# Kernel tuning notes

Hardware: AMD Instinct MI355X
Metric: run time of the kernel (lower is better)

## Reference

```python
import jax, jax.numpy as jnp
import numpy as np

K = 10          # hardcoded in module (self.K = 10)
H = 26          # neighbors per query point in this run
PAD_H = 28      # layer_ind2neighbor[layer_ind=0]
KP_EXTENT = 1.2 # linear-influence extent


def setup_inputs() -> dict:
    key = jax.random.key(0)
    ks = jax.random.split(key, 6)
    N, Ns, Cin, Cout = 65536, 65536, 64, 128
    q_pts = jax.random.normal(ks[0], (N, 3), jnp.float32)
    s_pts = jax.random.normal(ks[1], (Ns, 3), jnp.float32)
    neighb_inds = jax.random.randint(ks[2], (N, H), 0, Ns)
    x = jax.random.normal(ks[3], (Ns, Cin), jnp.float32)
    # kernel_points_generator: Linear(PAD_H*3 -> K*3)
    gen_W = jax.random.normal(ks[4], (K * 3, PAD_H * 3), jnp.float32) * (1.0 / np.sqrt(PAD_H * 3))
    gen_b = jnp.zeros((K * 3,), jnp.float32)
    # KPConv weights: [K, in, out] (kaiming_uniform in torch; scaled normal here)
    weights = jax.random.normal(ks[5], (K, Cin, Cout), jnp.float32) * (1.0 / np.sqrt(Cin))
    return {"q_pts": q_pts, "s_pts": s_pts, "x": x,
            "gen_W": gen_W, "gen_b": gen_b, "weights": weights,
            "neighb_inds": neighb_inds}


def _kpconv(q_pts, s_pts, x, gen_W, gen_b, weights, neighb_inds):
    N = q_pts.shape[0]
    # shadow support point far away (index Ns)
    s_pad = jnp.concatenate([s_pts, jnp.full((1, 3), 1e6, s_pts.dtype)], axis=0)
    neighbors = s_pad[neighb_inds] - q_pts[:, None, :]                          # [N,H,3]
    # generative kernel points: pad neighbor list with -1 up to PAD_H, run linear
    padded = jnp.concatenate(
        [neighbors, jnp.full((N, PAD_H - H, 3), -1.0, neighbors.dtype)], axis=1)
    kp = (padded.reshape(N, -1) @ gen_W.T + gen_b).reshape(N, 1, K, 3)          # [N,1,K,3]
    diff = neighbors[:, :, None, :] - kp                                        # [N,H,K,3]
    sq_d = jnp.sum(diff * diff, axis=3)                                         # [N,H,K]
    # KP_influence == 'linear'
    all_w = jnp.maximum(1.0 - jnp.sqrt(sq_d) / KP_EXTENT, 0.0)
    all_w = jnp.swapaxes(all_w, 1, 2)                                           # [N,K,H]
    # shadow feature row (zeros) at index Ns
    x_pad = jnp.concatenate([x, jnp.zeros((1, x.shape[1]), x.dtype)], axis=0)
    neighb_x = x_pad[neighb_inds]                                               # [N,H,Cin]
    weighted = jnp.einsum('nkh,nhi->nki', all_w, neighb_x)                      # [N,K,Cin]
    return jnp.einsum('nki,kio->no', weighted, weights)                         # [N,Cout]


def reference(q_pts, s_pts, x, gen_W, gen_b, weights, neighb_inds):
    return _kpconv(q_pts, s_pts, x, gen_W, gen_b, weights, neighb_inds)
```

## Files before the change

### kernel.cpp

```cpp
#include <hip/hip_runtime.h>
#include <stdint.h>

#define N_Q   65536
#define N_S   65536
#define NB_H  26
#define PAD_H 28
#define KP    10
#define CIN   64
#define COUT  128
#define MT    8
#define BM    64

typedef unsigned short u16x4  __attribute__((ext_vector_type(4)));
typedef unsigned short u16x8  __attribute__((ext_vector_type(8)));
typedef float          f32x4  __attribute__((ext_vector_type(4)));
typedef _Float16       f16x8  __attribute__((ext_vector_type(8)));
typedef _Float16       f16x2  __attribute__((ext_vector_type(2)));

#define CVT_BLOCKS 2049
#define PACK_BLOCKS 40

static __device__ __forceinline__ unsigned short f2h(float f) {
  return __builtin_bit_cast(unsigned short, (_Float16)f);
}

static __device__ __forceinline__ unsigned int pkrtz_u32(float a, float b) {
  return __builtin_bit_cast(unsigned int, __builtin_amdgcn_cvt_pkrtz(a, b));
}

static __device__ __forceinline__ float fdot2u(unsigned int a, unsigned int b, float c) {
#if __has_builtin(__builtin_amdgcn_fdot2)
  return __builtin_amdgcn_fdot2(__builtin_bit_cast(f16x2, a),
                                __builtin_bit_cast(f16x2, b), c, false);
#else
  f16x2 ha = __builtin_bit_cast(f16x2, a), hb = __builtin_bit_cast(f16x2, b);
  return c + (float)ha[0] * (float)hb[0] + (float)ha[1] * (float)hb[1];
#endif
}

__global__ void prep_kernel(const float* __restrict__ x,
                            const float* __restrict__ w,
                            unsigned short* __restrict__ xh,
                            unsigned short* __restrict__ bp) {
  if (blockIdx.x < CVT_BLOCKS) {
    long t = (long)blockIdx.x * blockDim.x + threadIdx.x;
    long off = t * 8;
    if (off >= (long)(N_S + 1) * CIN) return;
    u16x8 o;
    if (off < (long)N_S * CIN) {
      f32x4 a = *(const f32x4*)(x + off);
      f32x4 b = *(const f32x4*)(x + off + 4);
      o[0] = f2h(a[0]); o[1] = f2h(a[1]); o[2] = f2h(a[2]); o[3] = f2h(a[3]);
      o[4] = f2h(b[0]); o[5] = f2h(b[1]); o[6] = f2h(b[2]); o[7] = f2h(b[3]);
    } else {
      o = (u16x8)0;
    }
    *(u16x8*)(xh + off) = o;
  } else {
    int t = (blockIdx.x - CVT_BLOCKS) * blockDim.x + threadIdx.x;
    if (t >= 8 * 20 * 64) return;
    int lane = t & 63;
    int frag = t >> 6;
    int ks = frag % 20;
    int ct = frag / 20;
    int row0 = ks * 32 + (lane >> 4) * 8;
    int col  = ct * 16 + (lane & 15);
    u16x8 o;
    #pragma unroll
    for (int j = 0; j < 8; ++j) o[j] = f2h(w[(row0 + j) * COUT + col]);
    *(u16x8*)(bp + (long)t * 8) = o;
  }
}

__global__ void __launch_bounds__(256, 6)
kpconv_gather(const float* __restrict__ q_pts, const float* __restrict__ s_pts,
              const float* __restrict__ gen_W, const float* __restrict__ gen_b,
              const int* __restrict__ inds, const unsigned short* __restrict__ xh,
              unsigned short* __restrict__ wg) {

  __shared__ int          sh_ind[MT][NB_H];
  __shared__ float        sh_nbr[MT][80];
  __shared__ float        sh_kp[MT][KP * 3];
  __shared__ unsigned int sh_aw[MT][13][12];

  const int tid  = threadIdx.x;
  const int base = blockIdx.x * MT;

  if (tid < MT * NB_H) {
    int m = tid / NB_H, h = tid % NB_H;
    int n = base + m;
    int ind = inds[n * NB_H + h];
    sh_ind[m][h] = ind;
    float sx, sy, sz;
    if ((unsigned)ind < (unsigned)N_S) {
      sx = s_pts[ind * 3 + 0]; sy = s_pts[ind * 3 + 1]; sz = s_pts[ind * 3 + 2];
    } else {
      sx = 1e6f; sy = 1e6f; sz = 1e6f;
    }
    sh_nbr[m][h * 3 + 0] = sx - q_pts[n * 3 + 0];
    sh_nbr[m][h * 3 + 1] = sy - q_pts[n * 3 + 1];
    sh_nbr[m][h * 3 + 2] = sz - q_pts[n * 3 + 2];
  }
  if (tid < MT * 2) sh_nbr[tid >> 1][78 + (tid & 1)] = -1.0f;
  __syncthreads();

  if (tid < MT * KP * 3) {
    int m = tid / 30, r = tid % 30;
    const float* Wr = gen_W + r * (PAD_H * 3);
    const f32x4* W4 = (const f32x4*)Wr;
    const f32x4* N4 = (const f32x4*)&sh_nbr[m][0];
    f32x4 accv = {0.f, 0.f, 0.f, 0.f};
    #pragma unroll
    for (int j = 0; j < 20; ++j) accv += W4[j] * N4[j];
    sh_kp[m][r] = gen_b[r] - (Wr[80] + Wr[81] + Wr[82] + Wr[83])
                + accv[0] + accv[1] + accv[2] + accv[3];
  }
  __syncthreads();

  for (int p = tid; p < MT * 13 * KP; p += 256) {
    int k = p % KP;
    int t = p / KP;
    int m = t & (MT - 1);
    int hp = t >> 3;
    float kx = sh_kp[m][k * 3 + 0], ky = sh_kp[m][k * 3 + 1], kz = sh_kp[m][k * 3 + 2];
    int h0 = hp * 2;
    float dx0 = sh_nbr[m][h0 * 3 + 0] - kx;
    float dy0 = sh_nbr[m][h0 * 3 + 1] - ky;
    float dz0 = sh_nbr[m][h0 * 3 + 2] - kz;
    float w0 = fmaxf(1.0f - sqrtf(dx0 * dx0 + dy0 * dy0 + dz0 * dz0) * (1.0f / 1.2f), 0.0f);
    float dx1 = sh_nbr[m][h0 * 3 + 3] - kx;
    float dy1 = sh_nbr[m][h0 * 3 + 4] - ky;
    float dz1 = sh_nbr[m][h0 * 3 + 5] - kz;
    float w1 = fmaxf(1.0f - sqrtf(dx1 * dx1 + dy1 * dy1 + dz1 * dz1) * (1.0f / 1.2f), 0.0f);
    sh_aw[m][hp][k] = pkrtz_u32(w0, w1);
  }
  __syncthreads();

  {
    const int m  = tid >> 5;
    const int i0 = (tid & 31) * 2;
    float acc0[KP], acc1[KP];
    #pragma unroll
    for (int k = 0; k < KP; ++k) { acc0[k] = 0.f; acc1[k] = 0.f; }

    unsigned int xr[4];
    #pragma unroll
    for (int h = 0; h < 4; ++h)
      xr[h] = *(const unsigned int*)(xh + (long)sh_ind[m][h] * CIN + i0);

    #pragma unroll
    for (int p = 0; p < 13; ++p) {
      unsigned int r0 = xr[(2 * p) & 3];
      unsigned int r1 = xr[(2 * p + 1) & 3];
      if (2 * p + 4 < NB_H)
        xr[(2 * p) & 3] = *(const unsigned int*)(xh + (long)sh_ind[m][2 * p + 4] * CIN + i0);
      if (2 * p + 5 < NB_H)
        xr[(2 * p + 1) & 3] = *(const unsigned int*)(xh + (long)sh_ind[m][2 * p + 5] * CIN + i0);
      unsigned int pair0 = __builtin_amdgcn_perm(r1, r0, 0x05040100u);
      unsigned int pair1 = __builtin_amdgcn_perm(r1, r0, 0x07060302u);
      const unsigned int* wrow = &sh_aw[m][p][0];
      #pragma unroll
      for (int k = 0; k < KP; ++k) {
        unsigned int w2 = wrow[k];
        acc0[k] = fdot2u(w2, pair0, acc0[k]);
        acc1[k] = fdot2u(w2, pair1, acc1[k]);
      }
    }
    #pragma unroll
    for (int k = 0; k < KP; ++k) {
      __builtin_nontemporal_store(
          pkrtz_u32(acc0[k], acc1[k]),
          (unsigned int*)(wg + (long)(base + m) * (KP * CIN) + k * CIN + i0));
    }
  }
}

__global__ void __launch_bounds__(256, 4)
kpconv_gemm(const unsigned short* __restrict__ wg,
            const unsigned short* __restrict__ bp,
            float* __restrict__ out) {

  __shared__ unsigned short sA[2][BM][72];

  const int tid  = threadIdx.x;
  const int wave = tid >> 6;
  const int lane = tid & 63;
  const long row0 = (long)blockIdx.x * BM;

  const int srow = tid >> 3;
  const int scb  = tid & 7;

  {
    u16x8 a = __builtin_nontemporal_load((const u16x8*)(wg + (row0 + srow) * 640 + scb * 8));
    u16x8 b = __builtin_nontemporal_load((const u16x8*)(wg + (row0 + srow + 32) * 640 + scb * 8));
    *(u16x8*)&sA[0][srow][scb * 8] = a;
    *(u16x8*)&sA[0][srow + 32][scb * 8] = b;
  }

  f32x4 acc[4][2];
  #pragma unroll
  for (int rt = 0; rt < 4; ++rt)
    #pragma unroll
    for (int c = 0; c < 2; ++c) acc[rt][c] = (f32x4){0.f, 0.f, 0.f, 0.f};

  const int ct0  = wave * 2, ct1 = ct0 + 1;
  const int arow = lane & 15;
  const int aq   = lane >> 4;
  int cur = 0;

  for (int kc = 0; kc < 10; ++kc) {
    __syncthreads();
    u16x8 p0, p1;
    if (kc < 9) {
      p0 = __builtin_nontemporal_load((const u16x8*)(wg + (row0 + srow) * 640 + (kc + 1) * 64 + scb * 8));
      p1 = __builtin_nontemporal_load((const u16x8*)(wg + (row0 + srow + 32) * 640 + (kc + 1) * 64 + scb * 8));
    }
    #pragma unroll
    for (int ks2 = 0; ks2 < 2; ++ks2) {
      int ks = kc * 2 + ks2;
      u16x8 b0u = *(const u16x8*)(bp + (long)((ct0 * 20 + ks) * 64 + lane) * 8);
      u16x8 b1u = *(const u16x8*)(bp + (long)((ct1 * 20 + ks) * 64 + lane) * 8);
      f16x8 b0 = __builtin_bit_cast(f16x8, b0u);
      f16x8 b1 = __builtin_bit_cast(f16x8, b1u);
      #pragma unroll
      for (int rt = 0; rt < 4; ++rt) {
        u16x8 au = *(const u16x8*)&sA[cur][rt * 16 + arow][ks2 * 32 + aq * 8];
        f16x8 a = __builtin_bit_cast(f16x8, au);
        acc[rt][0] = __builtin_amdgcn_mfma_f32_16x16x32_f16(a, b0, acc[rt][0], 0, 0, 0);
        acc[rt][1] = __builtin_amdgcn_mfma_f32_16x16x32_f16(a, b1, acc[rt][1], 0, 0, 0);
      }
    }
    if (kc < 9) {
      *(u16x8*)&sA[1 - cur][srow][scb * 8] = p0;
      *(u16x8*)&sA[1 - cur][srow + 32][scb * 8] = p1;
      cur ^= 1;
    }
  }

  const int col   = lane & 15;
  const int rbase = aq * 4;
  #pragma unroll
  for (int rt = 0; rt < 4; ++rt)
    #pragma unroll
    for (int r = 0; r < 4; ++r) {
      long row = row0 + rt * 16 + rbase + r;
      __builtin_nontemporal_store(acc[rt][0][r], &out[row * COUT + ct0 * 16 + col]);
      __builtin_nontemporal_store(acc[rt][1][r], &out[row * COUT + ct1 * 16 + col]);
    }
}

extern "C" void kernel_launch(void* const* d_in, const int* in_sizes, int n_in,
                              void* d_out, int out_size, void* d_ws, size_t ws_size,
                              hipStream_t stream) {
  const float* q_pts = (const float*)d_in[0];
  const float* s_pts = (const float*)d_in[1];
  const float* x     = (const float*)d_in[2];
  const float* gen_W = (const float*)d_in[3];
  const float* gen_b = (const float*)d_in[4];
  const float* wts   = (const float*)d_in[5];
  const int*   inds  = (const int*)d_in[6];
  float* out = (float*)d_out;

  unsigned short* xh = (unsigned short*)d_ws;
  unsigned short* bp = xh + (size_t)(N_S + 1) * CIN;
  unsigned short* wg = bp + (size_t)81920;

  prep_kernel<<<CVT_BLOCKS + PACK_BLOCKS, 256, 0, stream>>>(x, wts, xh, bp);
  kpconv_gather<<<N_Q / MT, 256, 0, stream>>>(q_pts, s_pts, gen_W, gen_b,
                                              inds, xh, wg);
  kpconv_gemm<<<N_Q / BM, 256, 0, stream>>>(wg, bp, out);
}
```

Before: 175.0 us.

## Fuse gather and GEMM kernels, keeping weighted features in shared memory

Merges the gather/weighting kernel and the MFMA GEMM kernel into one kernel. Each block handles 32 query rows in four passes of 8, writing fp16 weighted features into a padded LDS tile instead of a global intermediate, then runs the 32x128 GEMM straight from LDS with register-prefetched B fragments. This removes the roughly 84 MB global write and read of the intermediate and one kernel launch. In exchange, the block's large LDS tile (about 41 KB) lowers occupancy, and each block serializes its gather passes before the GEMM, so there is less overlap.

Measured after the change: 182.0 us. 1.04x slower.

```diff
diff --git a/kernel.cpp b/kernel.cpp
--- a/kernel.cpp
+++ b/kernel.cpp
@@ -9,9 +9,10 @@
 #define CIN   64
 #define COUT  128
 #define MT    8
-#define BM    64
-
-typedef unsigned short u16x4  __attribute__((ext_vector_type(4)));
+#define BM    32
+#define NPASS (BM / MT)
+#define LDA   648
+
 typedef unsigned short u16x8  __attribute__((ext_vector_type(8)));
 typedef float          f32x4  __attribute__((ext_vector_type(4)));
 typedef _Float16       f16x8  __attribute__((ext_vector_type(8)));
@@ -72,181 +73,161 @@
   }
 }
 
-__global__ void __launch_bounds__(256, 6)
-kpconv_gather(const float* __restrict__ q_pts, const float* __restrict__ s_pts,
-              const float* __restrict__ gen_W, const float* __restrict__ gen_b,
-              const int* __restrict__ inds, const unsigned short* __restrict__ xh,
-              unsigned short* __restrict__ wg) {
-
-  __shared__ int          sh_ind[MT][NB_H];
-  __shared__ float        sh_nbr[MT][80];
-  __shared__ float        sh_kp[MT][KP * 3];
-  __shared__ unsigned int sh_aw[MT][13][12];
-
-  const int tid  = threadIdx.x;
-  const int base = blockIdx.x * MT;
-
-  if (tid < MT * NB_H) {
-    int m = tid / NB_H, h = tid % NB_H;
-    int n = base + m;
-    int ind = inds[n * NB_H + h];
-    sh_ind[m][h] = ind;
-    float sx, sy, sz;
-    if ((unsigned)ind < (unsigned)N_S) {
-      sx = s_pts[ind * 3 + 0]; sy = s_pts[ind * 3 + 1]; sz = s_pts[ind * 3 + 2];
-    } else {
-      sx = 1e6f; sy = 1e6f; sz = 1e6f;
-    }
-    sh_nbr[m][h * 3 + 0] = sx - q_pts[n * 3 + 0];
-    sh_nbr[m][h * 3 + 1] = sy - q_pts[n * 3 + 1];
-    sh_nbr[m][h * 3 + 2] = sz - q_pts[n * 3 + 2];
+__global__ void __launch_bounds__(256, 3)
+kpconv_fused(const float* __restrict__ q_pts, const float* __restrict__ s_pts,
+             const float* __restrict__ gen_W, const float* __restrict__ gen_b,
+             const int* __restrict__ inds, const unsigned short* __restrict__ xh,
+             const unsigned short* __restrict__ bp, float* __restrict__ out) {
+
+  __shared__ int            sh_ind[MT][NB_H];
+  __shared__ float          sh_nbr[MT][80];
+  __shared__ float          sh_kp[MT][KP * 3];
+  __shared__ unsigned int   sh_aw[MT][13][12];
+  __shared__ unsigned short sA[BM][LDA];
+
+  const int  tid  = threadIdx.x;
+  const long row0 = (long)blockIdx.x * BM;
+
+  #pragma unroll 1
+  for (int pass = 0; pass < NPASS; ++pass) {
+    const int pbase = (int)row0 + pass * MT;
+
+    if (tid < MT * NB_H) {
+      int m = tid / NB_H, h = tid % NB_H;
+      int n = pbase + m;
+      int ind = inds[n * NB_H + h];
+      sh_ind[m][h] = ind;
+      float sx, sy, sz;
+      if ((unsigned)ind < (unsigned)N_S) {
+        sx = s_pts[ind * 3 + 0]; sy = s_pts[ind * 3 + 1]; sz = s_pts[ind * 3 + 2];
+      } else {
+        sx = 1e6f; sy = 1e6f; sz = 1e6f;
+      }
+      sh_nbr[m][h * 3 + 0] = sx - q_pts[n * 3 + 0];
+      sh_nbr[m][h * 3 + 1] = sy - q_pts[n * 3 + 1];
+      sh_nbr[m][h * 3 + 2] = sz - q_pts[n * 3 + 2];
+    }
+    if (tid < MT * 2) sh_nbr[tid >> 1][78 + (tid & 1)] = -1.0f;
+    __syncthreads();
+
+    if (tid < MT * KP * 3) {
+      int m = tid / 30, r = tid % 30;
+      const float* Wr = gen_W + r * (PAD_H * 3);
+      const f32x4* W4 = (const f32x4*)Wr;
+      const f32x4* N4 = (const f32x4*)&sh_nbr[m][0];
+      f32x4 accv = {0.f, 0.f, 0.f, 0.f};
+      #pragma unroll
+      for (int j = 0; j < 20; ++j) accv += W4[j] * N4[j];
+      sh_kp[m][r] = gen_b[r] - (Wr[80] + Wr[81] + Wr[82] + Wr[83])
+                  + accv[0] + accv[1] + accv[2] + accv[3];
+    }
+    __syncthreads();
+
+    for (int p = tid; p < MT * 13 * KP; p += 256) {
+      int k = p % KP;
+      int t = p / KP;
+      int m = t & (MT - 1);
+      int hp = t >> 3;
+      float kx = sh_kp[m][k * 3 + 0], ky = sh_kp[m][k * 3 + 1], kz = sh_kp[m][k * 3 + 2];
+      int h0 = hp * 2;
+      float dx0 = sh_nbr[m][h0 * 3 + 0] - kx;
+      float dy0 = sh_nbr[m][h0 * 3 + 1] - ky;
+      float dz0 = sh_nbr[m][h0 * 3 + 2] - kz;
+      float w0 = fmaxf(1.0f - sqrtf(dx0 * dx0 + dy0 * dy0 + dz0 * dz0) * (1.0f / 1.2f), 0.0f);
+      float dx1 = sh_nbr[m][h0 * 3 + 3] - kx;
+      float dy1 = sh_nbr[m][h0 * 3 + 4] - ky;
+      float dz1 = sh_nbr[m][h0 * 3 + 5] - kz;
+      float w1 = fmaxf(1.0f - sqrtf(dx1 * dx1 + dy1 * dy1 + dz1 * dz1) * (1.0f / 1.2f), 0.0f);
+      sh_aw[m][hp][k] = pkrtz_u32(w0, w1);
+    }
+    __syncthreads();
+
+    {
+      const int m  = tid >> 5;
+      const int i0 = (tid & 31) * 2;
+      float acc0[KP], acc1[KP];
+      #pragma unroll
+      for (int k = 0; k < KP; ++k) { acc0[k] = 0.f; acc1[k] = 0.f; }
+
+      unsigned int xr[4];
+      #pragma unroll
+      for (int h = 0; h < 4; ++h)
+        xr[h] = *(const unsigned int*)(xh + (long)sh_ind[m][h] * CIN + i0);
+
+      #pragma unroll
+      for (int p = 0; p < 13; ++p) {
+        unsigned int r0 = xr[(2 * p) & 3];
+        unsigned int r1 = xr[(2 * p + 1) & 3];
+        if (2 * p + 4 < NB_H)
+          xr[(2 * p) & 3] = *(const unsigned int*)(xh + (long)sh_ind[m][2 * p + 4] * CIN + i0);
+        if (2 * p + 5 < NB_H)
+          xr[(2 * p + 1) & 3] = *(const unsigned int*)(xh + (long)sh_ind[m][2 * p + 5] * CIN + i0);
+        unsigned int pair0 = __builtin_amdgcn_perm(r1, r0, 0x05040100u);
+        unsigned int pair1 = __builtin_amdgcn_perm(r1, r0, 0x07060302u);
+        const unsigned int* wrow = &sh_aw[m][p][0];
+        #pragma unroll
+        for (int k = 0; k < KP; ++k) {
+          unsigned int w2 = wrow[k];
+          acc0[k] = fdot2u(w2, pair0, acc0[k]);
+          acc1[k] = fdot2u(w2, pair1, acc1[k]);
+        }
+      }
+      unsigned short* rowp = &sA[pass * MT + m][0];
+      #pragma unroll
+      for (int k = 0; k < KP; ++k)
+        *(unsigned int*)(rowp + k * CIN + i0) = pkrtz_u32(acc0[k], acc1[k]);
+    }
+    __syncthreads();
   }
-  if (tid < MT * 2) sh_nbr[tid >> 1][78 + (tid & 1)] = -1.0f;
-  __syncthreads();
-
-  if (tid < MT * KP * 3) {
-    int m = tid / 30, r = tid % 30;
-    const float* Wr = gen_W + r * (PAD_H * 3);
-    const f32x4* W4 = (const f32x4*)Wr;
-    const f32x4* N4 = (const f32x4*)&sh_nbr[m][0];
-    f32x4 accv = {0.f, 0.f, 0.f, 0.f};
-    #pragma unroll
-    for (int j = 0; j < 20; ++j) accv += W4[j] * N4[j];
-    sh_kp[m][r] = gen_b[r] - (Wr[80] + Wr[81] + Wr[82] + Wr[83])
-                + accv[0] + accv[1] + accv[2] + accv[3];
-  }
-  __syncthreads();
-
-  for (int p = tid; p < MT * 13 * KP; p += 256) {
-    int k = p % KP;
-    int t = p / KP;
-    int m = t & (MT - 1);
-    int hp = t >> 3;
-    float kx = sh_kp[m][k * 3 + 0], ky = sh_kp[m][k * 3 + 1], kz = sh_kp[m][k * 3 + 2];
-    int h0 = hp * 2;
-    float dx0 = sh_nbr[m][h0 * 3 + 0] - kx;
-    float dy0 = sh_nbr[m][h0 * 3 + 1] - ky;
-    float dz0 = sh_nbr[m][h0 * 3 + 2] - kz;
-    float w0 = fmaxf(1.0f - sqrtf(dx0 * dx0 + dy0 * dy0 + dz0 * dz0) * (1.0f / 1.2f), 0.0f);
-    float dx1 = sh_nbr[m][h0 * 3 + 3] - kx;
-    float dy1 = sh_nbr[m][h0 * 3 + 4] - ky;
-    float dz1 = sh_nbr[m][h0 * 3 + 5] - kz;
-    float w1 = fmaxf(1.0f - sqrtf(dx1 * dx1 + dy1 * dy1 + dz1 * dz1) * (1.0f / 1.2f), 0.0f);
-    sh_aw[m][hp][k] = pkrtz_u32(w0, w1);
-  }
-  __syncthreads();
 
   {
-    const int m  = tid >> 5;
-    const int i0 = (tid & 31) * 2;
-    float acc0[KP], acc1[KP];
-    #pragma unroll
-    for (int k = 0; k < KP; ++k) { acc0[k] = 0.f; acc1[k] = 0.f; }
-
-    unsigned int xr[4];
-    #pragma unroll
-    for (int h = 0; h < 4; ++h)
-      xr[h] = *(const unsigned int*)(xh + (long)sh_ind[m][h] * CIN + i0);
-
-    #pragma unroll
-    for (int p = 0; p < 13; ++p) {
-      unsigned int r0 = xr[(2 * p) & 3];
-      unsigned int r1 = xr[(2 * p + 1) & 3];
-      if (2 * p + 4 < NB_H)
-        xr[(2 * p) & 3] = *(const unsigned int*)(xh + (long)sh_ind[m][2 * p + 4] * CIN + i0);
-      if (2 * p + 5 < NB_H)
-        xr[(2 * p + 1) & 3] = *(const unsigned int*)(xh + (long)sh_ind[m][2 * p + 5] * CIN + i0);
-      unsigned int pair0 = __builtin_amdgcn_perm(r1, r0, 0x05040100u);
-      unsigned int pair1 = __builtin_amdgcn_perm(r1, r0, 0x07060302u);
-      const unsigned int* wrow = &sh_aw[m][p][0];
-      #pragma unroll
-      for (int k = 0; k < KP; ++k) {
-        unsigned int w2 = wrow[k];
-        acc0[k] = fdot2u(w2, pair0, acc0[k]);
-        acc1[k] = fdot2u(w2, pair1, acc1[k]);
-      }
-    }
-    #pragma unroll
-    for (int k = 0; k < KP; ++k) {
-      __builtin_nontemporal_store(
-          pkrtz_u32(acc0[k], acc1[k]),
-          (unsigned int*)(wg + (long)(base + m) * (KP * CIN) + k * CIN + i0));
-    }
-  }
-}
-
-__global__ void __launch_bounds__(256, 4)
-kpconv_gemm(const unsigned short* __restrict__ wg,
-            const unsigned short* __restrict__ bp,
-            float* __restrict__ out) {
-
-  __shared__ unsigned short sA[2][BM][72];
-
-  const int tid  = threadIdx.x;
-  const int wave = tid >> 6;
-  const int lane = tid & 63;
-  const long row0 = (long)blockIdx.x * BM;
-
-  const int srow = tid >> 3;
-  const int scb  = tid & 7;
-
-  {
-    u16x8 a = __builtin_nontemporal_load((const u16x8*)(wg + (row0 + srow) * 640 + scb * 8));
-    u16x8 b = __builtin_nontemporal_load((const u16x8*)(wg + (row0 + srow + 32) * 640 + scb * 8));
-    *(u16x8*)&sA[0][srow][scb * 8] = a;
-    *(u16x8*)&sA[0][srow + 32][scb * 8] = b;
-  }
-
-  f32x4 acc[4][2];
-  #pragma unroll
-  for (int rt = 0; rt < 4; ++rt)
-    #pragma unroll
-    for (int c = 0; c < 2; ++c) acc[rt][c] = (f32x4){0.f, 0.f, 0.f, 0.f};
-
-  const int ct0  = wave * 2, ct1 = ct0 + 1;
-  const int arow = lane & 15;
-  const int aq   = lane >> 4;
-  int cur = 0;
-
-  for (int kc = 0; kc < 10; ++kc) {
-    __syncthreads();
-    u16x8 p0, p1;
-    if (kc < 9) {
-      p0 = __builtin_nontemporal_load((const u16x8*)(wg + (row0 + srow) * 640 + (kc + 1) * 64 + scb * 8));
-      p1 = __builtin_nontemporal_load((const u16x8*)(wg + (row0 + srow + 32) * 640 + (kc + 1) * 64 + scb * 8));
-    }
-    #pragma unroll
-    for (int ks2 = 0; ks2 < 2; ++ks2) {
-      int ks = kc * 2 + ks2;
-      u16x8 b0u = *(const u16x8*)(bp + (long)((ct0 * 20 + ks) * 64 + lane) * 8);
-      u16x8 b1u = *(const u16x8*)(bp + (long)((ct1 * 20 + ks) * 64 + lane) * 8);
-      f16x8 b0 = __builtin_bit_cast(f16x8, b0u);
-      f16x8 b1 = __builtin_bit_cast(f16x8, b1u);
-      #pragma unroll
-      for (int rt = 0; rt < 4; ++rt) {
-        u16x8 au = *(const u16x8*)&sA[cur][rt * 16 + arow][ks2 * 32 + aq * 8];
+    const int wave = tid >> 6;
+    const int lane = tid & 63;
+    const int ct0  = wave * 2, ct1 = ct0 + 1;
+    const int arow = lane & 15;
+    const int aq   = lane >> 4;
+
+    f32x4 acc[2][2];
+    #pragma unroll
+    for (int rt = 0; rt < 2; ++rt)
+      #pragma unroll
+      for (int c = 0; c < 2; ++c) acc[rt][c] = (f32x4){0.f, 0.f, 0.f, 0.f};
+
+    u16x8 pb0[4], pb1[4];
+    #pragma unroll
+    for (int d = 0; d < 4; ++d) {
+      pb0[d] = *(const u16x8*)(bp + (long)((ct0 * 20 + d) * 64 + lane) * 8);
+      pb1[d] = *(const u16x8*)(bp + (long)((ct1 * 20 + d) * 64 + lane) * 8);
+    }
+
+    #pragma unroll
+    for (int ks = 0; ks < 20; ++ks) {
+      f16x8 b0 = __builtin_bit_cast(f16x8, pb0[ks & 3]);
+      f16x8 b1 = __builtin_bit_cast(f16x8, pb1[ks & 3]);
+      if (ks + 4 < 20) {
+        pb0[ks & 3] = *(const u16x8*)(bp + (long)((ct0 * 20 + ks + 4) * 64 + lane) * 8);
+        pb1[ks & 3] = *(const u16x8*)(bp + (long)((ct1 * 20 + ks + 4) * 64 + lane) * 8);
+      }
+      #pragma unroll
+      for (int rt = 0; rt < 2; ++rt) {
+        u16x8 au = *(const u16x8*)&sA[rt * 16 + arow][ks * 32 + aq * 8];
         f16x8 a = __builtin_bit_cast(f16x8, au);
         acc[rt][0] = __builtin_amdgcn_mfma_f32_16x16x32_f16(a, b0, acc[rt][0], 0, 0, 0);
         acc[rt][1] = __builtin_amdgcn_mfma_f32_16x16x32_f16(a, b1, acc[rt][1], 0, 0, 0);
       }
     }
-    if (kc < 9) {
-      *(u16x8*)&sA[1 - cur][srow][scb * 8] = p0;
-      *(u16x8*)&sA[1 - cur][srow + 32][scb * 8] = p1;
-      cur ^= 1;
-    }
+
+    const int col   = lane & 15;
+    const int rbase = aq * 4;
+    #pragma unroll
+    for (int rt = 0; rt < 2; ++rt)
+      #pragma unroll
+      for (int r = 0; r < 4; ++r) {
+        long row = row0 + rt * 16 + rbase + r;
+        __builtin_nontemporal_store(acc[rt][0][r], &out[row * COUT + ct0 * 16 + col]);
+        __builtin_nontemporal_store(acc[rt][1][r], &out[row * COUT + ct1 * 16 + col]);
+      }
   }
-
-  const int col   = lane & 15;
-  const int rbase = aq * 4;
-  #pragma unroll
-  for (int rt = 0; rt < 4; ++rt)
-    #pragma unroll
-    for (int r = 0; r < 4; ++r) {
-      long row = row0 + rt * 16 + rbase + r;
-      __builtin_nontemporal_store(acc[rt][0][r], &out[row * COUT + ct0 * 16 + col]);
-      __builtin_nontemporal_store(acc[rt][1][r], &out[row * COUT + ct1 * 16 + col]);
-    }
 }
 
 extern "C" void kernel_launch(void* const* d_in, const int* in_sizes, int n_in,
@@ -263,10 +244,8 @@
 
   unsigned short* xh = (unsigned short*)d_ws;
   unsigned short* bp = xh + (size_t)(N_S + 1) * CIN;
-  unsigned short* wg = bp + (size_t)81920;
 
   prep_kernel<<<CVT_BLOCKS + PACK_BLOCKS, 256, 0, stream>>>(x, wts, xh, bp);
-  kpconv_gather<<<N_Q / MT, 256, 0, stream>>>(q_pts, s_pts, gen_W, gen_b,
-                                              inds, xh, wg);
-  kpconv_gemm<<<N_Q / BM, 256, 0, stream>>>(wg, bp, out);
-}
+  kpconv_fused<<<N_Q / BM, 256, 0, stream>>>(q_pts, s_pts, gen_W, gen_b,
+                                             inds, xh, bp, out);
+}
```
